# Performance work log

Measured on AMD Instinct MI355X. Metric: run time of the kernel, lower is better.

## Reference

```python
import jax, jax.numpy as jnp
import numpy as np

NATTRS, NOBJS = 115, 245
N_NODES = NATTRS + NOBJS            # 360
FEAT = 512                          # graph embedding dim
HID = 2048                          # graph_encoder_layers[0]
NODE_DIM = 512                      # hparam.node_dim
EMB = 800                           # shared_emb_dim
IMG = 512                           # resnet18 feat dim
E = 1262                            # n train pairs (edges)
B = 256                             # batch
K = NATTRS - 1                      # negatives per sample (open-world)


def _l2(x):
    # F.normalize(..., dim=-1), eps=1e-12
    return x / jnp.clip(jnp.linalg.norm(x, axis=-1, keepdims=True), 1e-12)


def setup_inputs() -> dict:
    key = jax.random.key(0)
    ks = jax.random.split(key, 32)
    rn = lambda k, s, sc=0.02: jax.random.normal(k, s, dtype=jnp.float32) * sc
    ri = lambda k, s, hi: jax.random.randint(k, s, 0, hi, dtype=jnp.int64)
    return {
        "nodes": rn(ks[0], (N_NODES, FEAT), 1.0),
        "s_img": rn(ks[1], (B, IMG), 1.0),
        "t_img": rn(ks[2], (B, IMG), 1.0),
        # SAGEConv 1: FEAT -> HID ; SAGEConv 2: HID -> NODE_DIM
        "Wl1": rn(ks[3], (FEAT, HID)), "Wr1": rn(ks[4], (FEAT, HID)), "b1": jnp.zeros((HID,), jnp.float32),
        "Wl2": rn(ks[5], (HID, NODE_DIM)), "Wr2": rn(ks[6], (HID, NODE_DIM)), "b2": jnp.zeros((NODE_DIM,), jnp.float32),
        # pair_fc: 2*NODE_DIM -> 1000 -> EMB (norm_output)
        "Wp1": rn(ks[7], (2 * NODE_DIM, 1000)), "bp1": jnp.zeros((1000,), jnp.float32),
        "Wp2": rn(ks[8], (1000, EMB)), "bp2": jnp.zeros((EMB,), jnp.float32),
        # img_fc: IMG -> 800 -> 1000 -> EMB (norm_output)
        "Wi1": rn(ks[9], (IMG, 800)), "bi1": jnp.zeros((800,), jnp.float32),
        "Wi2": rn(ks[10], (800, 1000)), "bi2": jnp.zeros((1000,), jnp.float32),
        "Wi3": rn(ks[11], (1000, EMB)), "bi3": jnp.zeros((EMB,), jnp.float32),
        # compo_fc: IMG+EMB -> 800 -> 1000 -> EMB (norm_output)
        "Wc1": rn(ks[12], (IMG + EMB, 800)), "bc1": jnp.zeros((800,), jnp.float32),
        "Wc2": rn(ks[13], (800, 1000)), "bc2": jnp.zeros((1000,), jnp.float32),
        "Wc3": rn(ks[14], (1000, EMB)), "bc3": jnp.zeros((EMB,), jnp.float32),
        # graph / index data (train_pair_edges = [attr_idx; obj_idx], no offset, as in source)
        "edge_src": ri(ks[15], (E,), NATTRS),
        "edge_dst": ri(ks[16], (E,), NOBJS),
        "t_attr_ids": ri(ks[17], (B,), NATTRS),
        "obj_ids": ri(ks[18], (B,), NOBJS),
        "neg_attr_ids": ri(ks[19], (B, K), NATTRS),
        "nattrs": NATTRS,
    }


def reference(nodes, s_img, t_img,
              Wl1, Wr1, b1, Wl2, Wr2, b2,
              Wp1, bp1, Wp2, bp2,
              Wi1, bi1, Wi2, bi2, Wi3, bi3,
              Wc1, bc1, Wc2, bc2, Wc3, bc3,
              edge_src, edge_dst, t_attr_ids, obj_ids, neg_attr_ids, nattrs):
    N = nodes.shape[0]

    def sage(x, Wl, Wr, b):
        # PyG SAGEConv (mean aggr): lin_l(mean_{j->i} x_j) + lin_r(x_i) + bias
        cnt = jax.ops.segment_sum(jnp.ones(edge_dst.shape, x.dtype), edge_dst, num_segments=N)
        agg = jax.ops.segment_sum(x[edge_src], edge_dst, num_segments=N) / jnp.clip(cnt, 1.0)[:, None]
        return agg @ Wl + x @ Wr + b

    h = jax.nn.relu(sage(nodes, Wl1, Wr1, b1))          # [N, HID]
    z = sage(h, Wl2, Wr2, b2)                            # [N, NODE_DIM]

    def pair_fc(p):
        hh = jax.nn.relu(p @ Wp1 + bp1)
        return _l2(hh @ Wp2 + bp2)

    def mlp3(x, W1, c1, W2, c2, W3, c3):
        hh = jax.nn.relu(x @ W1 + c1)
        hh = jax.nn.relu(hh @ W2 + c2)
        return _l2(hh @ W3 + c3)

    obj_nodes = z[nattrs + obj_ids]                      # [B, NODE_DIM]
    t_pair = pair_fc(jnp.concatenate([z[t_attr_ids], obj_nodes], -1))   # [B, EMB]
    theta = mlp3(jnp.concatenate([s_img, t_pair], -1), Wc1, bc1, Wc2, bc2, Wc3, bc3)  # [B, EMB]
    targets = mlp3(t_img, Wi1, bi1, Wi2, bi2, Wi3, bi3)  # [B, EMB]

    # batched negative pairs (the per-sample loop, fused into one gather + batched MLP)
    neg_attr = z[neg_attr_ids]                           # [B, K, NODE_DIM]
    Bn, Kn = neg_attr.shape[0], neg_attr.shape[1]
    obj_b = jnp.broadcast_to(obj_nodes[:, None, :], neg_attr.shape)
    neg_pair = pair_fc(jnp.concatenate([neg_attr, obj_b], -1))          # [B, K, EMB]
    s_img_b = jnp.broadcast_to(s_img[:, None, :], (Bn, Kn, s_img.shape[1]))
    neg = mlp3(jnp.concatenate([s_img_b, neg_pair], -1), Wc1, bc1, Wc2, bc2, Wc3, bc3)  # [B, K, EMB]
    return (theta, targets, neg)
```

## Files before the change

kernel.cpp:

```cpp
#include <hip/hip_runtime.h>


typedef unsigned short u16;
typedef __bf16 bf16x8 __attribute__((ext_vector_type(8)));
typedef float f32x4 __attribute__((ext_vector_type(4)));

__device__ inline u16 f2bf_u(float f) {
  union { float f; unsigned u; } a; a.f = f;
  unsigned u = a.u + 0x7fffu + ((a.u >> 16) & 1u);
  return (u16)(u >> 16);
}
__device__ inline float bf2f_u(u16 h) {
  union { unsigned u; float f; } a; a.u = ((unsigned)h) << 16; return a.f;
}

#define GLOAD16(gptr, lptr)                                                   \
  __builtin_amdgcn_global_load_lds(                                           \
      (__attribute__((address_space(1))) void*)(gptr),                        \
      (__attribute__((address_space(3))) void*)(lptr), 16, 0, 0)

#define BAR  __builtin_amdgcn_s_barrier()
#define LGKM0 asm volatile("s_waitcnt lgkmcnt(0)" ::: "memory")
#define VMC4 asm volatile("s_waitcnt vmcnt(4)" ::: "memory")
#define VMC0 asm volatile("s_waitcnt vmcnt(0)" ::: "memory")

struct Panel {
  const u16* A; int lda;
  const u16* B; int ldb;
  const float* bias; int biasN;
  int N; int nK;
  void* out; int ldc;
  const float* rsVec;
  const float* addS;
  int gx;
  int rowG0;
};

template <int MODE>
__global__ __launch_bounds__(256, 4) void gemm128(
    Panel p0, Panel p1, int c0,
    float* __restrict__ rsPart, int rsLd,
    float* __restrict__ cTheta, float* __restrict__ cNeg, float* __restrict__ cTgt) {
  __shared__ u16 As[2][4096];
  __shared__ u16 Bs[2][4096];

  const int nwg = gridDim.x;
  const int orig = blockIdx.x;
  const int q = nwg >> 3, r = nwg & 7, xcd = orig & 7;
  const int basewg = (xcd < r) ? xcd * (q + 1) : r * (q + 1) + (xcd - r) * q;
  const int wg = basewg + (orig >> 3);

  Panel P; int pby, pbx;
  if (wg < c0) { P = p0; pby = wg / p0.gx; pbx = wg - pby * p0.gx; }
  else { P = p1; const int w2 = wg - c0; pby = w2 / p1.gx; pbx = w2 - pby * p1.gx; }
  const int m0 = pby << 7, n0 = pbx << 7;

  const int tid = threadIdx.x;
  const int wave = tid >> 6, lane = tid & 63;
  const int lr = lane & 15, lg = lane >> 4;
  const int wr = wave >> 1, wc = wave & 1;

  f32x4 acc[4][4] = {};

  const int r0 = tid >> 2, sc0 = tid & 3;
  const size_t aOff  = (size_t)(m0 + r0) * P.lda + ((sc0 ^ ((r0 >> 1) & 3)) << 3);
  const size_t aOff1 = (size_t)(m0 + r0 + 64) * P.lda + ((sc0 ^ (((r0 + 64) >> 1) & 3)) << 3);
  const size_t bOff  = (size_t)(n0 + r0) * P.ldb + ((sc0 ^ ((r0 >> 1) & 3)) << 3);
  const size_t bOff1 = (size_t)(n0 + r0 + 64) * P.ldb + ((sc0 ^ (((r0 + 64) >> 1) & 3)) << 3);
  const int lL = (r0 * 4 + sc0) << 4;

  auto stage = [&](int kt, int b) {
    const int k0 = kt << 5;
    GLOAD16(P.A + aOff + k0, (char*)As[b] + lL);
    GLOAD16(P.A + aOff1 + k0, (char*)As[b] + lL + 4096);
    GLOAD16(P.B + bOff + k0, (char*)Bs[b] + lL);
    GLOAD16(P.B + bOff1 + k0, (char*)Bs[b] + lL + 4096);
  };

  const int nK = P.nK;
  stage(0, 0);
  for (int kt = 0; kt < nK; ++kt) {
    const int cb = kt & 1;
    if (kt + 1 < nK) { stage(kt + 1, cb ^ 1); VMC4; }
    else { VMC0; }
    BAR;

    bf16x8 af[4], bv[4];
#pragma unroll
    for (int m = 0; m < 4; ++m) {
      const int row = (wr << 6) + (m << 4) + lr;
      af[m] = *(const bf16x8*)(&As[cb][row * 32 + ((lg ^ ((row >> 1) & 3)) << 3)]);
    }
#pragma unroll
    for (int n = 0; n < 4; ++n) {
      const int row = (wc << 6) + (n << 4) + lr;
      bv[n] = *(const bf16x8*)(&Bs[cb][row * 32 + ((lg ^ ((row >> 1) & 3)) << 3)]);
    }
#pragma unroll
    for (int m = 0; m < 4; ++m)
#pragma unroll
      for (int n = 0; n < 4; ++n)
        acc[m][n] = __builtin_amdgcn_mfma_f32_16x16x32_bf16(af[m], bv[n], acc[m][n], 0, 0, 0);

    LGKM0;
    BAR;
  }

  const int gcb = n0 + (wc << 6);
  const int grb = m0 + (wr << 6) + (lg << 2);
#pragma unroll
  for (int m = 0; m < 4; ++m) {
#pragma unroll
    for (int rr = 0; rr < 4; ++rr) {
      const int grow = grb + (m << 4) + rr;
      const int growG = P.rowG0 + grow;
      float ss = 0.f;
      float rs = 1.f;
      const float* Sp = nullptr;
      if (MODE == 0) {
        if (P.rsVec) rs = P.rsVec[growG];
        if (P.addS) {
          int bv2 = (growG < 256) ? growG : (growG - 256) / 114;
          Sp = P.addS + (size_t)bv2 * 4096;
        }
      }
#pragma unroll
      for (int n = 0; n < 4; ++n) {
        const int gc = gcb + (n << 4) + lr;
        if (gc >= P.N) continue;
        float v = acc[m][n][rr];
        if (MODE == 0) {
          v *= rs;
          if (gc < P.biasN) v += P.bias[gc];
          if (Sp) v += Sp[gc];
          v = fmaxf(v, 0.f);
          ((u16*)P.out)[(size_t)grow * P.ldc + gc] = f2bf_u(v);
        } else if (MODE == 1) {
          if (gc < P.biasN) v += P.bias[gc];
          ((u16*)P.out)[(size_t)grow * P.ldc + gc] = f2bf_u(v);
          ss += v * v;
        } else {
          if (gc < P.biasN) v += P.bias[gc];
          float* op = (growG < 256) ? cTheta + (size_t)growG * 800
                    : (growG < 29440) ? cNeg + (size_t)(growG - 256) * 800
                                      : cTgt + (size_t)(growG - 29440) * 800;
          op[gc] = v;
          ss += v * v;
        }
      }
      if (MODE == 1 || MODE == 3) {
        ss += __shfl_xor(ss, 1); ss += __shfl_xor(ss, 2);
        ss += __shfl_xor(ss, 4); ss += __shfl_xor(ss, 8);
        if (lr == 0) rsPart[(size_t)((pbx << 1) + wc) * rsLd + growG] = ss;
      }
    }
  }
}

template <int STORE>
__global__ __launch_bounds__(256) void gemm_atom(
    const u16* __restrict__ A, int lda, const u16* __restrict__ Bt, int ldb,
    int N, int nK, int ktChunk, float* __restrict__ Cf, int ldc, int zStride) {
  __shared__ u16 As[2][4096];
  __shared__ u16 Bs[2][4096];
  const int tid = threadIdx.x;
  const int wave = tid >> 6, lane = tid & 63;
  const int lr = lane & 15, lg = lane >> 4;
  const int wr = wave >> 1, wc = wave & 1;
  const int m0 = blockIdx.y << 7, n0 = blockIdx.x << 7;

  f32x4 acc[4][4] = {};

  const size_t aOff  = (size_t)(m0 + (tid >> 2)) * lda + ((tid & 3) << 3);
  const size_t aOff1 = aOff + (size_t)64 * lda;
  const size_t bOff  = (size_t)(n0 + (tid >> 2)) * ldb + ((tid & 3) << 3);
  const size_t bOff1 = bOff + (size_t)64 * ldb;

  const int kt0 = blockIdx.z * ktChunk;
  int ktEnd = kt0 + ktChunk; if (ktEnd > nK) ktEnd = nK;

  auto stage = [&](int kt, int b) {
    const int k0 = kt << 5;
    u16* Ad = &As[b][wave << 9];
    u16* Bd = &Bs[b][wave << 9];
    GLOAD16(A + aOff + k0, Ad);
    GLOAD16(A + aOff1 + k0, Ad + 2048);
    GLOAD16(Bt + bOff + k0, Bd);
    GLOAD16(Bt + bOff1 + k0, Bd + 2048);
  };

  if (kt0 < ktEnd) stage(kt0, 0);
  for (int kt = kt0; kt < ktEnd; ++kt) {
    const int cb = (kt - kt0) & 1;
    if (kt + 1 < ktEnd) {
      stage(kt + 1, cb ^ 1);
      VMC4;
    } else {
      VMC0;
    }
    BAR;
    asm volatile("" ::: "memory");

    bf16x8 af[4], bvv[4];
#pragma unroll
    for (int m = 0; m < 4; ++m)
      af[m] = *(const bf16x8*)(&As[cb][(((wr << 6) + (m << 4) + lr) << 5) + (lg << 3)]);
#pragma unroll
    for (int n = 0; n < 4; ++n)
      bvv[n] = *(const bf16x8*)(&Bs[cb][(((wc << 6) + (n << 4) + lr) << 5) + (lg << 3)]);
#pragma unroll
    for (int m = 0; m < 4; ++m)
#pragma unroll
      for (int n = 0; n < 4; ++n)
        acc[m][n] = __builtin_amdgcn_mfma_f32_16x16x32_bf16(af[m], bvv[n], acc[m][n], 0, 0, 0);

    asm volatile("s_waitcnt lgkmcnt(0)" ::: "memory");
    BAR;
    asm volatile("" ::: "memory");
  }

  float* out = STORE ? Cf : (Cf + (size_t)blockIdx.z * zStride);
  const int gcb = n0 + (wc << 6);
  const int grb = m0 + (wr << 6) + (lg << 2);
#pragma unroll
  for (int m = 0; m < 4; ++m)
#pragma unroll
    for (int rr = 0; rr < 4; ++rr) {
      const int grow = grb + (m << 4) + rr;
#pragma unroll
      for (int n = 0; n < 4; ++n) {
        const int gc = gcb + (n << 4) + lr;
        if (gc < N) out[(size_t)grow * ldc + gc] = acc[m][n][rr];
      }
    }
}

struct PK {
  const float* srcA; const float* srcB; u16* dst;
  int splitK, Ktot, Ksrc, Nsrc, srcLd, dstLd, Npad, nTiles, tile0;
};
struct PKs { PK j[12]; };

#define PREP_PACK_TILES 4992

__global__ __launch_bounds__(256) void k_prep(
    PKs J,
    const int* __restrict__ es, const int* __restrict__ ed,
    const float* __restrict__ nodes,
    const float* __restrict__ t_img, const float* __restrict__ s_img,
    u16* __restrict__ Agp, u16* __restrict__ dstT, u16* __restrict__ dstS) {
  __shared__ float t[64][65];
  int b = blockIdx.x;
  const int tid = threadIdx.x;

  if (b < PREP_PACK_TILES) {
    int ji = 0;
#pragma unroll
    for (int jj = 1; jj < 12; ++jj)
      if (b >= J.j[jj].tile0) ji = jj;
    PK job = J.j[ji];
    const int local = b - job.tile0;
    const int kTile = local / job.nTiles, nTile = local - kTile * job.nTiles;
    const int k0 = kTile << 6, n0 = nTile << 6;
    const int blk = k0 / job.Ktot;
    const int km0 = k0 - blk * job.Ktot;
    const float* src = (km0 < job.splitK)
        ? job.srcA + (size_t)km0 * job.srcLd
        : job.srcB + (size_t)(km0 - job.splitK) * job.srcLd;
    const bool lo = (blk == 2);

    const int rr = tid >> 4, cc = (tid & 15) << 2;
    const bool interior = (km0 + 64 <= job.Ksrc) && (n0 + 64 <= job.Nsrc);
#pragma unroll
    for (int i = 0; i < 4; ++i) {
      const int row = rr + (i << 4);
      float4 v;
      if (interior) {
        v = *(const float4*)(src + (size_t)row * job.srcLd + n0 + cc);
      } else {
        v.x = v.y = v.z = v.w = 0.f;
        if (km0 + row < job.Ksrc) {
          const float* sr = src + (size_t)row * job.srcLd + n0 + cc;
          if (n0 + cc + 0 < job.Nsrc) v.x = sr[0];
          if (n0 + cc + 1 < job.Nsrc) v.y = sr[1];
          if (n0 + cc + 2 < job.Nsrc) v.z = sr[2];
          if (n0 + cc + 3 < job.Nsrc) v.w = sr[3];
        }
      }
      t[row][cc] = v.x; t[row][cc + 1] = v.y; t[row][cc + 2] = v.z; t[row][cc + 3] = v.w;
    }
    __syncthreads();
    const int nr = tid >> 2, kc = (tid & 3) << 4;
    if (n0 + nr < job.Npad) {
      u16 o[16] __attribute__((aligned(16)));
#pragma unroll
      for (int jx = 0; jx < 16; ++jx) {
        float x = t[kc + jx][nr];
        u16 hb = f2bf_u(x);
        o[jx] = lo ? f2bf_u(x - bf2f_u(hb)) : hb;
      }
      u16* dp = job.dst + (size_t)(n0 + nr) * job.dstLd + k0 + kc;
      *(uint4*)dp = *(const uint4*)&o[0];
      *(uint4*)(dp + 8) = *(const uint4*)&o[8];
    }
    return;
  }
  b -= PREP_PACK_TILES;
  if (b < 384) {
    const int node = b;
    const int c = tid * 2;
    u16* row = Agp + (size_t)node * 3072;
    if (node >= 360) {
#pragma unroll
      for (int bb = 0; bb < 3; ++bb) { row[bb * 1024 + c] = 0; row[bb * 1024 + c + 1] = 0;
                                       row[bb * 1024 + 512 + c] = 0; row[bb * 1024 + 512 + c + 1] = 0; }
      return;
    }
    float a0 = 0.f, a1 = 0.f, cnt = 0.f;
    for (int e = 0; e < 1262; ++e) {
      if (ed[e] == node) {
        const float* xr = nodes + (size_t)es[e] * 512;
        a0 += xr[c]; a1 += xr[c + 1]; cnt += 1.f;
      }
    }
    float inv = 1.f / fmaxf(cnt, 1.f);
    a0 *= inv; a1 *= inv;
    float x0 = nodes[(size_t)node * 512 + c], x1 = nodes[(size_t)node * 512 + c + 1];
    u16 ah0 = f2bf_u(a0), ah1 = f2bf_u(a1);
    u16 al0 = f2bf_u(a0 - bf2f_u(ah0)), al1 = f2bf_u(a1 - bf2f_u(ah1));
    u16 xh0 = f2bf_u(x0), xh1 = f2bf_u(x1);
    u16 xl0 = f2bf_u(x0 - bf2f_u(xh0)), xl1 = f2bf_u(x1 - bf2f_u(xh1));
    row[c] = ah0; row[c + 1] = ah1; row[512 + c] = xh0; row[512 + c + 1] = xh1;
    row[1024 + c] = al0; row[1024 + c + 1] = al1; row[1536 + c] = xl0; row[1536 + c + 1] = xl1;
    row[2048 + c] = ah0; row[2048 + c + 1] = ah1; row[2560 + c] = xh0; row[2560 + c + 1] = xh1;
    return;
  }
  b -= 384;
  {
    const int idx = b * 256 + tid;
    const float* src = (idx < 32768) ? t_img : s_img;
    u16* dst = (idx < 32768) ? dstT : dstS;
    const int i = idx & 32767;
    float4 v = *(const float4*)(src + ((size_t)i << 2));
    ushort4 o;
    o.x = f2bf_u(v.x); o.y = f2bf_u(v.y); o.z = f2bf_u(v.z); o.w = f2bf_u(v.w);
    *(ushort4*)(dst + ((size_t)i << 2)) = o;
  }
}

__global__ void k_aggpack2(const int* __restrict__ es, const int* __restrict__ ed,
                           const float* __restrict__ Hf, u16* __restrict__ A2p) {
  const int node = blockIdx.x;
  const int c = threadIdx.x * 8;
  u16* row = A2p + (size_t)node * 12288;
  if (node >= 360) {
#pragma unroll
    for (int b = 0; b < 3; ++b)
      for (int j = 0; j < 8; ++j) { row[b * 4096 + c + j] = 0; row[b * 4096 + 2048 + c + j] = 0; }
    return;
  }
  float a[8] = {}; float cnt = 0.f;
  for (int e = 0; e < 1262; ++e) {
    if (ed[e] == node) {
      const float* hr = Hf + (size_t)es[e] * 2048 + c;
      float4 v0 = *(const float4*)hr, v1 = *(const float4*)(hr + 4);
      a[0] += v0.x; a[1] += v0.y; a[2] += v0.z; a[3] += v0.w;
      a[4] += v1.x; a[5] += v1.y; a[6] += v1.z; a[7] += v1.w;
      cnt += 1.f;
    }
  }
  float inv = 1.f / fmaxf(cnt, 1.f);
  const float* hx = Hf + (size_t)node * 2048 + c;
#pragma unroll
  for (int j = 0; j < 8; ++j) {
    float av = a[j] * inv, xv = hx[j];
    u16 ah = f2bf_u(av), xh = f2bf_u(xv);
    u16 al = f2bf_u(av - bf2f_u(ah)), xl = f2bf_u(xv - bf2f_u(xh));
    row[c + j] = ah; row[2048 + c + j] = xh;
    row[4096 + c + j] = al; row[6144 + c + j] = xl;
    row[8192 + c + j] = ah; row[10240 + c + j] = xh;
  }
}

__global__ void k_relu_bias_f32(const float* __restrict__ acc, const float* __restrict__ bias,
                                float* __restrict__ out, int N, int total, int nz, int zs) {
  int idx = blockIdx.x * 256 + threadIdx.x;
  if (idx >= total) return;
  float s = 0.f;
  for (int z = 0; z < nz; ++z) s += acc[(size_t)z * zs + idx];
  out[idx] = fmaxf(s + bias[idx % N], 0.f);
}
__global__ void k_bias_bf16(const float* __restrict__ acc, const float* __restrict__ bias,
                            u16* __restrict__ out, int N, int total, int nz, int zs) {
  int idx = blockIdx.x * 256 + threadIdx.x;
  if (idx >= total) return;
  float s = 0.f;
  for (int z = 0; z < nz; ++z) s += acc[(size_t)z * zs + idx];
  out[idx] = f2bf_u(s + bias[idx % N]);
}

__global__ void k_buildH1T1(const float* __restrict__ Facc,
                            const int* __restrict__ t_attr, const int* __restrict__ obj,
                            const int* __restrict__ negat, const float* __restrict__ bp1,
                            const float* __restrict__ bi1,
                            u16* __restrict__ H1, u16* __restrict__ T1) {
  int idx = blockIdx.x * 256 + threadIdx.x;
  if (idx >= 29696 * 128) return;
  int r = idx >> 7, ch = idx & 127, c = ch << 3;
  if (r < 29440) {
    u16* dst = H1 + ((size_t)r << 10) + c;
    if (c >= 1000) { ushort4 z = {0,0,0,0}; *(ushort4*)dst = z; *(ushort4*)(dst + 4) = z; return; }
    int a, o;
    if (r < 256) { a = t_attr[r]; o = obj[r]; }
    else { int rr = r - 256; a = negat[rr]; o = obj[rr / 114]; }
    const float* Fa = Facc + (size_t)a * 4096 + c;
    const float* Go = Facc + (size_t)(115 + o) * 4096 + 1024 + c;
    const float* Bp = bp1 + c;
    ushort4 o0, o1;
    float4 f0 = *(const float4*)Fa, f1 = *(const float4*)(Fa + 4);
    float4 g0 = *(const float4*)Go, g1 = *(const float4*)(Go + 4);
    float4 b0 = *(const float4*)Bp, b1 = *(const float4*)(Bp + 4);
    o0.x = f2bf_u(fmaxf(f0.x + g0.x + b0.x, 0.f));
    o0.y = f2bf_u(fmaxf(f0.y + g0.y + b0.y, 0.f));
    o0.z = f2bf_u(fmaxf(f0.z + g0.z + b0.z, 0.f));
    o0.w = f2bf_u(fmaxf(f0.w + g0.w + b0.w, 0.f));
    o1.x = f2bf_u(fmaxf(f1.x + g1.x + b1.x, 0.f));
    o1.y = f2bf_u(fmaxf(f1.y + g1.y + b1.y, 0.f));
    o1.z = f2bf_u(fmaxf(f1.z + g1.z + b1.z, 0.f));
    o1.w = f2bf_u(fmaxf(f1.w + g1.w + b1.w, 0.f));
    *(ushort4*)dst = o0; *(ushort4*)(dst + 4) = o1;
  } else {
    int rt = r - 29440;
    if (ch >= 104) return;
    u16* dst = T1 + (size_t)rt * 832 + c;
    if (c >= 800) { ushort4 z = {0,0,0,0}; *(ushort4*)dst = z; *(ushort4*)(dst + 4) = z; return; }
    const float* I1 = Facc + (size_t)(384 + rt) * 4096 + 2048 + c;
    const float* Bi = bi1 + c;
    float4 f0 = *(const float4*)I1, f1 = *(const float4*)(I1 + 4);
    float4 b0 = *(const float4*)Bi, b1 = *(const float4*)(Bi + 4);
    ushort4 o0, o1;
    o0.x = f2bf_u(fmaxf(f0.x + b0.x, 0.f)); o0.y = f2bf_u(fmaxf(f0.y + b0.y, 0.f));
    o0.z = f2bf_u(fmaxf(f0.z + b0.z, 0.f)); o0.w = f2bf_u(fmaxf(f0.w + b0.w, 0.f));
    o1.x = f2bf_u(fmaxf(f1.x + b1.x, 0.f)); o1.y = f2bf_u(fmaxf(f1.y + b1.y, 0.f));
    o1.z = f2bf_u(fmaxf(f1.z + b1.z, 0.f)); o1.w = f2bf_u(fmaxf(f1.w + b1.w, 0.f));
    *(ushort4*)dst = o0; *(ushort4*)(dst + 4) = o1;
  }
}

__global__ void k_rs(const float* __restrict__ part, int nrows, float* __restrict__ rs) {
  int idx = blockIdx.x * 256 + threadIdx.x;
  if (idx >= nrows) return;
  float s = 0.f;
#pragma unroll
  for (int i = 0; i < 14; ++i) s += part[(size_t)i * nrows + idx];
  rs[idx] = rsqrtf(fmaxf(s, 1e-24f));
}

__global__ void k_norm3c(float* __restrict__ cTheta, float* __restrict__ cNeg,
                         float* __restrict__ cTgt, const float* __restrict__ rsC) {
  int idx = blockIdx.x * 256 + threadIdx.x;
  if (idx >= 29696 * 200) return;
  int r = idx / 200, c = (idx - r * 200) << 2;
  float s = rsC[r];
  float* row = (r < 256) ? cTheta + (size_t)r * 800
             : (r < 29440) ? cNeg + (size_t)(r - 256) * 800
                           : cTgt + (size_t)(r - 29440) * 800;
  float4 v = *(float4*)(row + c);
  v.x *= s; v.y *= s; v.z *= s; v.w *= s;
  *(float4*)(row + c) = v;
}

extern "C" void kernel_launch(void* const* d_in, const int* in_sizes, int n_in,
                              void* d_out, int out_size, void* d_ws, size_t ws_size,
                              hipStream_t stream) {
  const float* nodes = (const float*)d_in[0];
  const float* s_img = (const float*)d_in[1];
  const float* t_img = (const float*)d_in[2];
  const float* Wl1 = (const float*)d_in[3];
  const float* Wr1 = (const float*)d_in[4];
  const float* b1  = (const float*)d_in[5];
  const float* Wl2 = (const float*)d_in[6];
  const float* Wr2 = (const float*)d_in[7];
  const float* b2  = (const float*)d_in[8];
  const float* Wp1 = (const float*)d_in[9];
  const float* bp1 = (const float*)d_in[10];
  const float* Wp2 = (const float*)d_in[11];
  const float* bp2 = (const float*)d_in[12];
  const float* Wi1 = (const float*)d_in[13];
  const float* bi1 = (const float*)d_in[14];
  const float* Wi2 = (const float*)d_in[15];
  const float* bi2 = (const float*)d_in[16];
  const float* Wi3 = (const float*)d_in[17];
  const float* bi3 = (const float*)d_in[18];
  const float* Wc1 = (const float*)d_in[19];
  const float* bc1 = (const float*)d_in[20];
  const float* Wc2 = (const float*)d_in[21];
  const float* bc2 = (const float*)d_in[22];
  const float* Wc3 = (const float*)d_in[23];
  const float* bc3 = (const float*)d_in[24];
  const int* e_src = (const int*)d_in[25];
  const int* e_dst = (const int*)d_in[26];
  const int* t_attr = (const int*)d_in[27];
  const int* obj    = (const int*)d_in[28];
  const int* negat  = (const int*)d_in[29];
  (void)in_sizes; (void)n_in; (void)out_size; (void)ws_size;

  float* out = (float*)d_out;
  float* cTheta = out;
  float* cTgt = out + 204800;
  float* cNeg = out + 409600;

  char* p = (char*)d_ws;
  auto alloc = [&](size_t bytes) -> void* {
    char* r = p; p += (bytes + 255) & ~(size_t)255; return (void*)r;
  };
  u16* W1t   = (u16*)alloc(2048ull * 3072 * 2);
  u16* W2t   = (u16*)alloc(512ull * 12288 * 2);
  u16* Wp2t  = (u16*)alloc(1024ull * 1024 * 2);
  u16* Wc1bt = (u16*)alloc(1024ull * 832 * 2);
  u16* Wc2t  = (u16*)alloc(1024ull * 896 * 2);
  u16* Wc3t  = (u16*)alloc(1024ull * 1024 * 2);
  u16* Wi2t  = (u16*)alloc(1024ull * 832 * 2);
  u16* Wi3t  = (u16*)alloc(1024ull * 1024 * 2);
  u16* Wcat  = (u16*)alloc(4096ull * 512 * 2);
  u16* Agp   = (u16*)alloc(384ull * 3072 * 2);
  float* Hacc = (float*)alloc(8ull * 384 * 2048 * 4);
  float* Hf   = (float*)alloc(384ull * 2048 * 4);
  u16* A2p   = (u16*)alloc(384ull * 12288 * 2);
  float* Zacc = (float*)alloc(16ull * 384 * 512 * 4);
  u16* A_cat = (u16*)alloc(896ull * 512 * 2);
  float* Facc = (float*)alloc(896ull * 4096 * 4);
  u16* T1    = (u16*)alloc(256ull * 832 * 2);
  u16* T2    = (u16*)alloc(256ull * 1024 * 2);
  float* rsqP16 = (float*)alloc(16ull * 29440 * 4);
  float* rsqC16 = (float*)alloc(16ull * 29696 * 4);
  float* rsP = (float*)alloc(29440ull * 4);
  float* rsC = (float*)alloc(29696ull * 4);
  u16* H1 = (u16*)alloc(29440ull * 1024 * 2);
  u16* X  = (u16*)alloc(29440ull * 832 * 2);
  u16* H3 = (u16*)alloc(29440ull * 1024 * 2);
  u16* H2 = H1;

  const int BIG = 1 << 28;
  {
    PKs J;
    J.j[0]  = {Wl1,             Wr1,  W1t,    512,  1024, 1024, 2048, 2048, 3072, 2048, 32, 0};
    J.j[1]  = {Wl2,             Wr2,  W2t,   2048,  4096, 4096,  512,  512, 12288, 512,  8, 1536};
    J.j[2]  = {Wp2,             Wp2,  Wp2t,   BIG,   BIG, 1000,  800,  800, 1024, 1024, 16, 3072};
    J.j[3]  = {Wc1 + 512 * 800, Wc1,  Wc1bt,  BIG,   BIG,  800,  800,  800,  832, 1024, 16, 3328};
    J.j[4]  = {Wc2,             Wc2,  Wc2t,   BIG,   BIG,  800, 1000, 1000,  896, 1024, 16, 3536};
    J.j[5]  = {Wc3,             Wc3,  Wc3t,   BIG,   BIG, 1000,  800,  800, 1024, 1024, 16, 3760};
    J.j[6]  = {Wi2,             Wi2,  Wi2t,   BIG,   BIG,  800, 1000, 1000,  832, 1024, 16, 4016};
    J.j[7]  = {Wi3,             Wi3,  Wi3t,   BIG,   BIG, 1000,  800,  800, 1024, 1024, 16, 4224};
    J.j[8]  = {Wp1,             Wp1,  Wcat,   BIG,   BIG,  512, 1000, 1000,  512, 1024, 16, 4480};
    J.j[9]  = {Wp1 + 512 * 1000, Wp1, Wcat + 1024 * 512, BIG, BIG, 512, 1000, 1000, 512, 1024, 16, 4608};
    J.j[10] = {Wi1,             Wi1,  Wcat + 2048 * 512, BIG, BIG, 512,  800,  800,  512, 1024, 16, 4736};
    J.j[11] = {Wc1,             Wc1,  Wcat + 3072 * 512, BIG, BIG, 512,  800,  800,  512, 1024, 16, 4864};
    k_prep<<<dim3(PREP_PACK_TILES + 384 + 256), 256, 0, stream>>>(
        J, e_src, e_dst, nodes, t_img, s_img,
        Agp, A_cat + 384 * 512, A_cat + 640 * 512);
  }

  gemm_atom<0><<<dim3(16, 3, 8), 256, 0, stream>>>(Agp, 3072, W1t, 3072, 2048, 96, 12,
                                                   Hacc, 2048, 384 * 2048);
  k_relu_bias_f32<<<dim3(384 * 2048 / 256), 256, 0, stream>>>(Hacc, b1, Hf, 2048,
                                                              384 * 2048, 8, 384 * 2048);
  k_aggpack2<<<dim3(384), 256, 0, stream>>>(e_src, e_dst, Hf, A2p);
  gemm_atom<0><<<dim3(4, 3, 16), 256, 0, stream>>>(A2p, 12288, W2t, 12288, 512, 384, 24,
                                                   Zacc, 512, 384 * 512);
  k_bias_bf16<<<dim3(384 * 512 / 256), 256, 0, stream>>>(Zacc, b2, A_cat, 512,
                                                         384 * 512, 16, 384 * 512);

  gemm_atom<1><<<dim3(32, 7, 1), 256, 0, stream>>>(A_cat, 512, Wcat, 512, 4096, 16, 16,
                                                   Facc, 4096, 0);
  k_buildH1T1<<<dim3(29696 * 128 / 256), 256, 0, stream>>>(Facc, t_attr, obj, negat,
                                                           bp1, bi1, H1, T1);

  {
    Panel s0{H1, 1024, Wp2t, 1024, bp2, 800, 832, 32, X, 832, nullptr, nullptr, 7, 0};
    gemm128<1><<<dim3(1610), 256, 0, stream>>>(s0, s0, 1 << 30, rsqP16, 29440,
                                               nullptr, nullptr, nullptr);
  }
  k_rs<<<dim3(115), 256, 0, stream>>>(rsqP16, 29440, rsP);

  {
    Panel s0{X, 832, Wc1bt, 832, bc1, 800, 896, 26, H2, 896, rsP,
             Facc + 640 * 4096 + 3072, 7, 0};
    Panel s1{T1, 832, Wi2t, 832, bi2, 1000, 1024, 26, T2, 1024, nullptr, nullptr, 8, 29440};
    gemm128<0><<<dim3(1626), 256, 0, stream>>>(s0, s1, 1610, nullptr, 0,
                                               nullptr, nullptr, nullptr);
  }
  {
    Panel s0{H2, 896, Wc2t, 896, bc2, 1000, 1024, 28, H3, 1024, nullptr, nullptr, 8, 0};
    gemm128<0><<<dim3(1840), 256, 0, stream>>>(s0, s0, 1 << 30, nullptr, 0,
                                               nullptr, nullptr, nullptr);
  }
  {
    Panel s0{H3, 1024, Wc3t, 1024, bc3, 800, 800, 32, nullptr, 800, nullptr, nullptr, 7, 0};
    Panel s1{T2, 1024, Wi3t, 1024, bi3, 800, 800, 32, nullptr, 800, nullptr, nullptr, 7, 29440};
    gemm128<3><<<dim3(1624), 256, 0, stream>>>(s0, s1, 1610, rsqC16, 29696,
                                               cTheta, cNeg, cTgt);
  }
  k_rs<<<dim3(116), 256, 0, stream>>>(rsqC16, 29696, rsC);
  k_norm3c<<<dim3((29696 * 200 + 255) / 256), 256, 0, stream>>>(cTheta, cNeg, cTgt, rsC);
}
```

Before: 665.4 us.

## Load B fragments directly from global into registers, bypassing LDS

The B tile is no longer staged through shared memory. Each wave now loads its B fragments straight from global memory into registers, double-buffered across k-steps, while A stays in LDS. This halves LDS usage and cuts LDS traffic, at the cost of more registers (occupancy hint lowered from 4 to 3) and duplicated global B reads across the two wave rows. The wait count is changed to match the six outstanding loads per step.

```diff
diff --git a/kernel.cpp b/kernel.cpp
--- a/kernel.cpp
+++ b/kernel.cpp
@@ -21,6 +21,7 @@
 
 #define BAR  __builtin_amdgcn_s_barrier()
 #define LGKM0 asm volatile("s_waitcnt lgkmcnt(0)" ::: "memory")
+#define VMC6 asm volatile("s_waitcnt vmcnt(6)" ::: "memory")
 #define VMC4 asm volatile("s_waitcnt vmcnt(4)" ::: "memory")
 #define VMC0 asm volatile("s_waitcnt vmcnt(0)" ::: "memory")
 
@@ -37,12 +38,11 @@
 };
 
 template <int MODE>
-__global__ __launch_bounds__(256, 4) void gemm128(
+__global__ __launch_bounds__(256, 3) void gemm128(
     Panel p0, Panel p1, int c0,
     float* __restrict__ rsPart, int rsLd,
     float* __restrict__ cTheta, float* __restrict__ cNeg, float* __restrict__ cTgt) {
   __shared__ u16 As[2][4096];
-  __shared__ u16 Bs[2][4096];
 
   const int nwg = gridDim.x;
   const int orig = blockIdx.x;
@@ -65,45 +65,58 @@
   const int r0 = tid >> 2, sc0 = tid & 3;
   const size_t aOff  = (size_t)(m0 + r0) * P.lda + ((sc0 ^ ((r0 >> 1) & 3)) << 3);
   const size_t aOff1 = (size_t)(m0 + r0 + 64) * P.lda + ((sc0 ^ (((r0 + 64) >> 1) & 3)) << 3);
-  const size_t bOff  = (size_t)(n0 + r0) * P.ldb + ((sc0 ^ ((r0 >> 1) & 3)) << 3);
-  const size_t bOff1 = (size_t)(n0 + r0 + 64) * P.ldb + ((sc0 ^ (((r0 + 64) >> 1) & 3)) << 3);
   const int lL = (r0 * 4 + sc0) << 4;
 
-  auto stage = [&](int kt, int b) {
+  auto stageA = [&](int kt, int b) {
     const int k0 = kt << 5;
     GLOAD16(P.A + aOff + k0, (char*)As[b] + lL);
     GLOAD16(P.A + aOff1 + k0, (char*)As[b] + lL + 4096);
-    GLOAD16(P.B + bOff + k0, (char*)Bs[b] + lL);
-    GLOAD16(P.B + bOff1 + k0, (char*)Bs[b] + lL + 4096);
   };
 
-  const int nK = P.nK;
-  stage(0, 0);
-  for (int kt = 0; kt < nK; ++kt) {
+  const u16* bBase = P.B + (size_t)(n0 + (wc << 6) + lr) * P.ldb + (lg << 3);
+  const size_t bStride16 = (size_t)16 * P.ldb;
+
+  auto loadB = [&](bf16x8 (&bv)[4], int kt) {
+    const int k0 = kt << 5;
+#pragma unroll
+    for (int nf = 0; nf < 4; ++nf)
+      bv[nf] = *(const bf16x8*)(bBase + (size_t)nf * bStride16 + k0);
+  };
+
+  auto iterBody = [&](int kt, bf16x8 (&bCur)[4], bf16x8 (&bNext)[4]) {
     const int cb = kt & 1;
-    if (kt + 1 < nK) { stage(kt + 1, cb ^ 1); VMC4; }
-    else { VMC0; }
+    if (kt + 1 < P.nK) {
+      stageA(kt + 1, cb ^ 1);
+      loadB(bNext, kt + 1);
+      VMC6;
+    } else {
+      VMC0;
+    }
     BAR;
 
-    bf16x8 af[4], bv[4];
+    bf16x8 af[4];
 #pragma unroll
     for (int m = 0; m < 4; ++m) {
       const int row = (wr << 6) + (m << 4) + lr;
       af[m] = *(const bf16x8*)(&As[cb][row * 32 + ((lg ^ ((row >> 1) & 3)) << 3)]);
     }
 #pragma unroll
-    for (int n = 0; n < 4; ++n) {
-      const int row = (wc << 6) + (n << 4) + lr;
-      bv[n] = *(const bf16x8*)(&Bs[cb][row * 32 + ((lg ^ ((row >> 1) & 3)) << 3)]);
-    }
-#pragma unroll
     for (int m = 0; m < 4; ++m)
 #pragma unroll
       for (int n = 0; n < 4; ++n)
-        acc[m][n] = __builtin_amdgcn_mfma_f32_16x16x32_bf16(af[m], bv[n], acc[m][n], 0, 0, 0);
+        acc[m][n] = __builtin_amdgcn_mfma_f32_16x16x32_bf16(af[m], bCur[n], acc[m][n], 0, 0, 0);
 
     LGKM0;
     BAR;
+  };
+
+  const int nK = P.nK;
+  bf16x8 bv0[4], bv1[4];
+  stageA(0, 0);
+  loadB(bv0, 0);
+  for (int kt = 0; kt < nK; kt += 2) {
+    iterBody(kt, bv0, bv1);
+    if (kt + 1 < nK) iterBody(kt + 1, bv1, bv0);
   }
 
   const int gcb = n0 + (wc << 6);
```

Measured after the change: 885.4 us. 1.33x slower.
